# Optimization experiments

Measured on AMD Instinct MI355X. Metric: run time of the kernel, lower is better.

The kernel has to match this reference:

```python
import jax, jax.numpy as jnp
from jax import lax
import numpy as np

WIDTH = 3.0        # tool half-width (voxels)
SIGMA = 1.0        # soft mask edge (voxels)
BLUR_SIGMA = 1.5   # post-deposit isotropic blur sigma (voxels)
EPS = 1e-8


def _gauss_blur(x, sigma):
    """Separable Gaussian blur over the last two axes of x: [B, X, Y]."""
    radius = int(3 * sigma)
    t = jnp.arange(-radius, radius + 1, dtype=x.dtype)
    k = jnp.exp(-0.5 * (t / sigma) ** 2)
    k = k / k.sum()
    x4 = x[:, None]                      # [B,1,X,Y] NCHW
    kh = k.reshape(1, 1, -1, 1)
    x4 = lax.conv_general_dilated(x4, kh, (1, 1), 'SAME')
    kw = k.reshape(1, 1, 1, -1)
    x4 = lax.conv_general_dilated(x4, kw, (1, 1), 'SAME')
    return x4[:, 0]


def setup_inputs() -> dict:
    key = jax.random.key(0)
    k1, k2, k3 = jax.random.split(key, 3)
    B, H, W = 16, 1024, 1024
    occ = jax.random.uniform(k1, (B, H, W), dtype=jnp.float32)
    # push start/end points well inside the grid (voxel coordinates)
    action_start = jax.random.uniform(k2, (B, 3), minval=200.0, maxval=800.0, dtype=jnp.float32)
    action_end = action_start + jax.random.uniform(k3, (B, 3), minval=-150.0, maxval=150.0, dtype=jnp.float32)
    return {"occ": occ, "action_start": action_start, "action_end": action_end}


def reference(occ, action_start, action_end):
    # coordinate-convention transpose (see SplatPushModel docs)
    rho = jnp.swapaxes(occ, 1, 2)            # [B, X, Y]
    B, X, Y = rho.shape
    p0 = action_start[:, :2]                 # [B,2]
    p1 = action_end[:, :2]                   # [B,2]

    d = p1 - p0
    L = jnp.sqrt(jnp.sum(d * d, axis=-1) + EPS)      # [B] segment length
    u = d / L[:, None]                               # unit push direction
    n = jnp.stack([-u[:, 1], u[:, 0]], axis=-1)      # unit normal

    gx = jnp.arange(X, dtype=rho.dtype)[None, :, None]   # [1,X,1]
    gy = jnp.arange(Y, dtype=rho.dtype)[None, None, :]   # [1,1,Y]
    bc = lambda v: v[:, None, None]                      # [B] -> [B,1,1]

    # --- swept band: soft distance-to-segment mask ---
    rx = gx - bc(p0[:, 0])
    ry = gy - bc(p0[:, 1])
    t = jnp.clip(rx * bc(u[:, 0]) + ry * bc(u[:, 1]), 0.0, L[:, None, None])
    dx = rx - t * bc(u[:, 0])
    dy = ry - t * bc(u[:, 1])
    dist = jnp.sqrt(dx * dx + dy * dy + EPS)
    swept = jax.nn.sigmoid((WIDTH - dist) / SIGMA)       # [B,X,Y]

    m_swept = jnp.sum(rho * swept, axis=(1, 2))          # [B] mass to move
    pile_depth = m_swept / (2.0 * WIDTH)                 # [B]

    # --- landing zone probe (rectangle past p1) ---
    qx = gx - bc(p1[:, 0])
    qy = gy - bc(p1[:, 1])
    s = qx * bc(u[:, 0]) + qy * bc(u[:, 1])              # along-direction coord
    r = qx * bc(n[:, 0]) + qy * bc(n[:, 1])              # perpendicular coord
    lat = jax.nn.sigmoid((WIDTH - jnp.abs(r)) / SIGMA)
    probe = jax.nn.sigmoid(s / SIGMA) * jax.nn.sigmoid((bc(pile_depth) - s) / SIGMA) * lat
    existing = jnp.sum(rho * probe, axis=(1, 2))         # [B]
    extra = existing / (2.0 * WIDTH)                     # [B] forward extension

    # --- deposit band, shifted forward by extra_depth ---
    dep_mask = (jax.nn.sigmoid((s - bc(extra)) / SIGMA)
                * jax.nn.sigmoid((bc(extra) + bc(pile_depth) - s) / SIGMA)
                * lat)
    dep_norm = m_swept / (jnp.sum(dep_mask, axis=(1, 2)) + EPS)
    dep = dep_mask * dep_norm[:, None, None]             # mass-conserving deposit

    if BLUR_SIGMA > 0:
        dep = _gauss_blur(dep, BLUR_SIGMA)

    rho_new = rho * (1.0 - swept) + dep
    return jnp.swapaxes(rho_new, 1, 2)
```

## Files before the change

kernel.cpp:

```cpp
#include <hip/hip_runtime.h>
#include <math.h>

#define BB    16
#define HH    1024
#define WW    1024
#define EPSF  1e-8f
#define RAD   4
#define MARG  24.f
#define WMAX  256
#define FW    (WMAX + 16)

struct BlurK { float k[9]; };

__device__ __forceinline__ float sigf(float z) {
    z = fmaxf(fminf(z, 40.f), -40.f);
    return 1.f / (1.f + __expf(-z));
}

struct Geom { float p0x, p0y, p1x, p1y, L, ux, uy; };

__device__ __forceinline__ Geom load_geom(const float* as, const float* ae, int b) {
    Geom g;
    g.p0x = as[3 * b];  g.p0y = as[3 * b + 1];
    g.p1x = ae[3 * b];  g.p1y = ae[3 * b + 1];
    float dx = g.p1x - g.p0x, dy = g.p1y - g.p0y;
    g.L  = sqrtf(dx * dx + dy * dy + EPSF);
    g.ux = dx / g.L;  g.uy = dy / g.L;
    return g;
}

__device__ __forceinline__ float sweptf(const Geom& g, float x, float y) {
    float rx = x - g.p0x, ry = y - g.p0y;
    float t  = fminf(fmaxf(rx * g.ux + ry * g.uy, 0.f), g.L);
    float dx = rx - t * g.ux, dy = ry - t * g.uy;
    float dist = sqrtf(dx * dx + dy * dy + EPSF);
    return sigf(3.f - dist);
}

__device__ __forceinline__ void slat(const Geom& g, float x, float y, float& s, float& lat) {
    float qx = x - g.p1x, qy = y - g.p1y;
    s = qx * g.ux + qy * g.uy;
    float r = qx * (-g.uy) + qy * g.ux;
    lat = sigf(3.f - fabsf(r));
}

__device__ __forceinline__ void capsule_bbox(const Geom& g, float m,
                                             int& x0, int& x1, int& y0, int& y1) {
    x0 = max(0, (int)floorf(fminf(g.p0x, g.p1x) - m));
    x1 = min(WW - 1, (int)ceilf(fmaxf(g.p0x, g.p1x) + m));
    y0 = max(0, (int)floorf(fminf(g.p0y, g.p1y) - m));
    y1 = min(HH - 1, (int)ceilf(fmaxf(g.p0y, g.p1y) + m));
}

__device__ __forceinline__ void strip_bbox(const Geom& g, float s0, float s1, float m,
                                           int& x0, int& x1, int& y0, int& y1) {
    float xmin = 1e9f, xmax = -1e9f, ymin = 1e9f, ymax = -1e9f;
    #pragma unroll
    for (int i = 0; i < 4; i++) {
        float s = (i & 1) ? s1 : s0;
        float r = (i & 2) ? m : -m;
        float x = g.p1x + s * g.ux - r * g.uy;
        float y = g.p1y + s * g.uy + r * g.ux;
        xmin = fminf(xmin, x); xmax = fmaxf(xmax, x);
        ymin = fminf(ymin, y); ymax = fmaxf(ymax, y);
    }
    x0 = max(0, (int)floorf(xmin)); x1 = min(WW - 1, (int)ceilf(xmax));
    y0 = max(0, (int)floorf(ymin)); y1 = min(HH - 1, (int)ceilf(ymax));
}

__device__ __forceinline__ float brb1024(float v, float* sm) {
    #pragma unroll
    for (int off = 32; off > 0; off >>= 1) v += __shfl_down(v, off);
    const int lane = threadIdx.x & 63, wid = threadIdx.x >> 6;
    if (lane == 0) sm[wid] = v;
    __syncthreads();
    float r = 0.f;
    #pragma unroll
    for (int i = 0; i < 16; i++) r += sm[i];
    __syncthreads();
    return r;
}

__global__ __launch_bounds__(1024)
void k_scalars(const float* __restrict__ occ, const float* __restrict__ as,
               const float* __restrict__ ae, float* __restrict__ sc) {
    const int b = blockIdx.x, tid = threadIdx.x;
    const int ty = tid >> 7, tx = tid & 127;
    __shared__ float sm[16];
    Geom g = load_geom(as, ae, b);
    const float* base = occ + ((size_t)b << 20);

    int x0, x1, y0, y1;
    capsule_bbox(g, MARG, x0, x1, y0, y1);
    float sum = 0.f;
    for (int y = y0 + ty; y <= y1; y += 8) {
        const float fy = (float)y;
        for (int x = x0 + tx; x <= x1; x += 128)
            sum += base[((size_t)y << 10) + x] * sweptf(g, (float)x, fy);
    }
    const float m_swept = brb1024(sum, sm);
    const float pile = m_swept * (1.f / 6.f);

    strip_bbox(g, -MARG, pile + MARG, MARG, x0, x1, y0, y1);
    sum = 0.f;
    for (int y = y0 + ty; y <= y1; y += 8) {
        const float fy = (float)y;
        for (int x = x0 + tx; x <= x1; x += 128) {
            float s, lat; slat(g, (float)x, fy, s, lat);
            sum += base[((size_t)y << 10) + x] * sigf(s) * sigf(pile - s) * lat;
        }
    }
    const float existing = brb1024(sum, sm);
    const float extra = existing * (1.f / 6.f);

    strip_bbox(g, extra - MARG, extra + pile + MARG, MARG, x0, x1, y0, y1);
    sum = 0.f;
    for (int y = y0 + ty; y <= y1; y += 8) {
        const float fy = (float)y;
        for (int x = x0 + tx; x <= x1; x += 128) {
            float s, lat; slat(g, (float)x, fy, s, lat);
            sum += sigf(s - extra) * sigf(extra + pile - s) * lat;
        }
    }
    const float summask = brb1024(sum, sm);

    if (tid == 0) {
        sc[b * 4 + 0] = pile;
        sc[b * 4 + 1] = extra;
        sc[b * 4 + 2] = m_swept / (summask + EPSF);
    }
}

__global__ __launch_bounds__(256)
void k_fused(const float* __restrict__ occ, const float* __restrict__ as,
             const float* __restrict__ ae, const float* __restrict__ sc,
             float* __restrict__ out, BlurK wk) {
    const int b = blockIdx.y, bx = blockIdx.x, tid = threadIdx.x;
    const float pile     = sc[b * 4 + 0];
    const float extra    = sc[b * 4 + 1];
    const float dep_norm = sc[b * 4 + 2];
    Geom g = load_geom(as, ae, b);

    const size_t ibase = (size_t)b << 20;
    const float4* src = (const float4*)(occ + ibase);
    float4*       dst = (float4*)(out + ibase);
    const int yb = bx * 8;
    const int base4 = bx * 2048 + tid;

    float4 v[8];
    #pragma unroll
    for (int k = 0; k < 8; k++) v[k] = src[base4 + k * 256];

    int cx0, cx1, cy0, cy1; capsule_bbox(g, MARG, cx0, cx1, cy0, cy1);
    const int x = tid << 2;
    if (x + 3 >= cx0 && x <= cx1) {
        #pragma unroll
        for (int k = 0; k < 8; k++) {
            const int y = yb + k;
            if (y >= cy0 && y <= cy1) {
                const float fy = (float)y, fx = (float)x;
                v[k].x *= 1.f - sweptf(g, fx + 0.f, fy);
                v[k].y *= 1.f - sweptf(g, fx + 1.f, fy);
                v[k].z *= 1.f - sweptf(g, fx + 2.f, fy);
                v[k].w *= 1.f - sweptf(g, fx + 3.f, fy);
            }
        }
    }

    int sx0, sx1, sy0, sy1;
    strip_bbox(g, extra - MARG, extra + pile + MARG, MARG, sx0, sx1, sy0, sy1);

    __shared__ float draw[16][FW];
    __shared__ float hb[16][WMAX];

    if (yb + 7 >= sy0 && yb <= sy1) {
        const int cxa = sx0 & ~3;
        for (int cx = cxa; cx <= sx1; cx += WMAX) {
            const int w = min(WMAX, sx1 - cx + 1);

            for (int i = tid; i < 16 * FW; i += 256) {
                const int ly = i / FW, lx = i - ly * FW;
                if (lx < w + 8) {
                    const int gy = yb - 4 + ly, gx = cx - 4 + lx;
                    float val = 0.f;
                    if ((unsigned)gx < WW && (unsigned)gy < HH) {
                        float s, lat; slat(g, (float)gx, (float)gy, s, lat);
                        val = sigf(s - extra) * sigf(extra + pile - s) * lat * dep_norm;
                    }
                    draw[ly][lx] = val;
                }
            }
            __syncthreads();

            for (int i = tid; i < 16 * WMAX; i += 256) {
                const int ly = i >> 8, lx = i & 255;
                if (lx < w) {
                    float acc = 0.f;
                    #pragma unroll
                    for (int j = 0; j < 9; j++) acc += wk.k[j] * draw[ly][lx + j];
                    hb[ly][lx] = acc;
                }
            }
            __syncthreads();

            for (int i = tid; i < 8 * WMAX; i += 256) {
                const int k = i >> 8, lx = i & 255;
                if (lx < w) {
                    float acc = 0.f;
                    #pragma unroll
                    for (int j = 0; j < 9; j++) acc += wk.k[j] * hb[k + j][lx];
                    draw[k][lx] = acc;
                }
            }
            __syncthreads();

            const int lx0 = (tid << 2) - cx;
            if (lx0 >= 0 && lx0 < w) {
                if (lx0 + 3 < w) {
                    #pragma unroll
                    for (int k = 0; k < 8; k++) {
                        const float4 vb = *(const float4*)&draw[k][lx0];
                        v[k].x += vb.x; v[k].y += vb.y; v[k].z += vb.z; v[k].w += vb.w;
                    }
                } else {
                    #pragma unroll
                    for (int k = 0; k < 8; k++)
                        for (int e = 0; e < 4; e++)
                            if (lx0 + e < w) (&v[k].x)[e] += draw[k][lx0 + e];
                }
            }
            __syncthreads();
        }
    }

    #pragma unroll
    for (int k = 0; k < 8; k++) dst[base4 + k * 256] = v[k];
}

extern "C" void kernel_launch(void* const* d_in, const int* in_sizes, int n_in,
                              void* d_out, int out_size, void* d_ws, size_t ws_size,
                              hipStream_t stream) {
    const float* occ = (const float*)d_in[0];
    const float* as  = (const float*)d_in[1];
    const float* ae  = (const float*)d_in[2];
    float* out = (float*)d_out;
    float* sc  = (float*)d_ws;

    BlurK wk;
    {
        float s = 0.f;
        for (int i = 0; i < 9; i++) {
            float t = (float)(i - RAD) / 1.5f;
            wk.k[i] = expf(-0.5f * t * t);
            s += wk.k[i];
        }
        for (int i = 0; i < 9; i++) wk.k[i] /= s;
    }

    k_scalars<<<dim3(BB), 1024, 0, stream>>>(occ, as, ae, sc);
    k_fused  <<<dim3(HH / 8, BB), 256, 0, stream>>>(occ, as, ae, sc, out, wk);
}
```

Baseline: 167.0 us.

## Tighten deposit blur x-range per row band and vectorize scalar reductions

In the fused kernel, each row band now computes the exact x-interval where the rotated deposit rectangle crosses its 16 halo rows, and only blurs that range. The blur tile width drops from 256 to 128 to cut padded work. In the scalar kernel, the swept and probe reductions now load occ as float4 and unroll four rows, exposing more memory-level parallelism. The intent is to skip blur work on the mostly-empty axis-aligned bounding box and to cut the latency-bound serial scalar kernel, at the cost of per-block interval math and more tile iterations.

```diff
diff --git a/kernel.cpp b/kernel.cpp
--- a/kernel.cpp
+++ b/kernel.cpp
@@ -7,8 +7,9 @@
 #define EPSF  1e-8f
 #define RAD   4
 #define MARG  24.f
-#define WMAX  256
+#define WMAX  128
 #define FW    (WMAX + 16)
+#define UNR   4
 
 struct BlurK { float k[9]; };
 
@@ -68,6 +69,14 @@
     y0 = max(0, (int)floorf(ymin)); y1 = min(HH - 1, (int)ceilf(ymax));
 }
 
+__device__ __forceinline__ bool ivx(float a, float A, float B, float& lo, float& hi) {
+    if (fabsf(a) < 1e-5f) return !(A > 0.f || B < 0.f);
+    float l = A / a, h = B / a;
+    if (a < 0.f) { float t = l; l = h; h = t; }
+    lo = fmaxf(lo, l); hi = fminf(hi, h);
+    return true;
+}
+
 __device__ __forceinline__ float brb1024(float v, float* sm) {
     #pragma unroll
     for (int off = 32; off > 0; off >>= 1) v += __shfl_down(v, off);
@@ -85,29 +94,72 @@
 void k_scalars(const float* __restrict__ occ, const float* __restrict__ as,
                const float* __restrict__ ae, float* __restrict__ sc) {
     const int b = blockIdx.x, tid = threadIdx.x;
-    const int ty = tid >> 7, tx = tid & 127;
+    const int tx4 = tid & 63;
+    const int ty  = tid >> 6;
     __shared__ float sm[16];
     Geom g = load_geom(as, ae, b);
-    const float* base = occ + ((size_t)b << 20);
+    const float4* src4 = (const float4*)(occ + ((size_t)b << 20));
 
     int x0, x1, y0, y1;
+
     capsule_bbox(g, MARG, x0, x1, y0, y1);
+    int c0 = x0 >> 2, c1 = x1 >> 2;
     float sum = 0.f;
-    for (int y = y0 + ty; y <= y1; y += 8) {
-        const float fy = (float)y;
-        for (int x = x0 + tx; x <= x1; x += 128)
-            sum += base[((size_t)y << 10) + x] * sweptf(g, (float)x, fy);
+    for (int cc = c0; cc <= c1; cc += 64) {
+        const int c = cc + tx4;
+        const bool cok = (c <= c1);
+        const float fx = (float)(c << 2);
+        for (int y = y0 + ty; y <= y1; y += 16 * UNR) {
+            float4 vv[UNR];
+            #pragma unroll
+            for (int j = 0; j < UNR; j++) {
+                const int yy = y + 16 * j;
+                vv[j] = (cok && yy <= y1) ? src4[yy * 256 + c]
+                                          : make_float4(0.f, 0.f, 0.f, 0.f);
+            }
+            #pragma unroll
+            for (int j = 0; j < UNR; j++) {
+                const int yy = y + 16 * j;
+                if (cok && yy <= y1) {
+                    const float fy = (float)yy;
+                    sum += vv[j].x * sweptf(g, fx + 0.f, fy);
+                    sum += vv[j].y * sweptf(g, fx + 1.f, fy);
+                    sum += vv[j].z * sweptf(g, fx + 2.f, fy);
+                    sum += vv[j].w * sweptf(g, fx + 3.f, fy);
+                }
+            }
+        }
     }
     const float m_swept = brb1024(sum, sm);
     const float pile = m_swept * (1.f / 6.f);
 
     strip_bbox(g, -MARG, pile + MARG, MARG, x0, x1, y0, y1);
+    c0 = x0 >> 2; c1 = x1 >> 2;
     sum = 0.f;
-    for (int y = y0 + ty; y <= y1; y += 8) {
-        const float fy = (float)y;
-        for (int x = x0 + tx; x <= x1; x += 128) {
-            float s, lat; slat(g, (float)x, fy, s, lat);
-            sum += base[((size_t)y << 10) + x] * sigf(s) * sigf(pile - s) * lat;
+    for (int cc = c0; cc <= c1; cc += 64) {
+        const int c = cc + tx4;
+        const bool cok = (c <= c1);
+        const float fx = (float)(c << 2);
+        for (int y = y0 + ty; y <= y1; y += 16 * UNR) {
+            float4 vv[UNR];
+            #pragma unroll
+            for (int j = 0; j < UNR; j++) {
+                const int yy = y + 16 * j;
+                vv[j] = (cok && yy <= y1) ? src4[yy * 256 + c]
+                                          : make_float4(0.f, 0.f, 0.f, 0.f);
+            }
+            #pragma unroll
+            for (int j = 0; j < UNR; j++) {
+                const int yy = y + 16 * j;
+                if (cok && yy <= y1) {
+                    const float fy = (float)yy;
+                    #pragma unroll
+                    for (int e = 0; e < 4; e++) {
+                        float s, lat; slat(g, fx + (float)e, fy, s, lat);
+                        sum += (&vv[j].x)[e] * sigf(s) * sigf(pile - s) * lat;
+                    }
+                }
+            }
         }
     }
     const float existing = brb1024(sum, sm);
@@ -115,11 +167,14 @@
 
     strip_bbox(g, extra - MARG, extra + pile + MARG, MARG, x0, x1, y0, y1);
     sum = 0.f;
-    for (int y = y0 + ty; y <= y1; y += 8) {
-        const float fy = (float)y;
-        for (int x = x0 + tx; x <= x1; x += 128) {
-            float s, lat; slat(g, (float)x, fy, s, lat);
-            sum += sigf(s - extra) * sigf(extra + pile - s) * lat;
+    {
+        const int tx = tid & 127, ty8 = tid >> 7;
+        for (int y = y0 + ty8; y <= y1; y += 8) {
+            const float fy = (float)y;
+            for (int x = x0 + tx; x <= x1; x += 128) {
+                float s, lat; slat(g, (float)x, fy, s, lat);
+                sum += sigf(s - extra) * sigf(extra + pile - s) * lat;
+            }
         }
     }
     const float summask = brb1024(sum, sm);
@@ -174,62 +229,77 @@
     __shared__ float hb[16][WMAX];
 
     if (yb + 7 >= sy0 && yb <= sy1) {
-        const int cxa = sx0 & ~3;
-        for (int cx = cxa; cx <= sx1; cx += WMAX) {
-            const int w = min(WMAX, sx1 - cx + 1);
-
-            for (int i = tid; i < 16 * FW; i += 256) {
-                const int ly = i / FW, lx = i - ly * FW;
-                if (lx < w + 8) {
-                    const int gy = yb - 4 + ly, gx = cx - 4 + lx;
-                    float val = 0.f;
-                    if ((unsigned)gx < WW && (unsigned)gy < HH) {
-                        float s, lat; slat(g, (float)gx, (float)gy, s, lat);
-                        val = sigf(s - extra) * sigf(extra + pile - s) * lat * dep_norm;
-                    }
-                    draw[ly][lx] = val;
-                }
-            }
-            __syncthreads();
-
-            for (int i = tid; i < 16 * WMAX; i += 256) {
-                const int ly = i >> 8, lx = i & 255;
-                if (lx < w) {
-                    float acc = 0.f;
-                    #pragma unroll
-                    for (int j = 0; j < 9; j++) acc += wk.k[j] * draw[ly][lx + j];
-                    hb[ly][lx] = acc;
-                }
-            }
-            __syncthreads();
-
-            for (int i = tid; i < 8 * WMAX; i += 256) {
-                const int k = i >> 8, lx = i & 255;
-                if (lx < w) {
-                    float acc = 0.f;
-                    #pragma unroll
-                    for (int j = 0; j < 9; j++) acc += wk.k[j] * hb[k + j][lx];
-                    draw[k][lx] = acc;
-                }
-            }
-            __syncthreads();
-
-            const int lx0 = (tid << 2) - cx;
-            if (lx0 >= 0 && lx0 < w) {
-                if (lx0 + 3 < w) {
-                    #pragma unroll
-                    for (int k = 0; k < 8; k++) {
-                        const float4 vb = *(const float4*)&draw[k][lx0];
-                        v[k].x += vb.x; v[k].y += vb.y; v[k].z += vb.z; v[k].w += vb.w;
-                    }
-                } else {
-                    #pragma unroll
-                    for (int k = 0; k < 8; k++)
-                        for (int e = 0; e < 4; e++)
-                            if (lx0 + e < w) (&v[k].x)[e] += draw[k][lx0 + e];
-                }
-            }
-            __syncthreads();
+        const float sA = extra - MARG, sB = extra + pile + MARG;
+        float xlo = 1e9f, xhi = -1e9f;
+        #pragma unroll
+        for (int r = 0; r < 16; r++) {
+            const float dy = (float)(yb - RAD + r) - g.p1y;
+            float lo = -1e9f, hi = 1e9f;
+            bool ok = ivx(g.ux, sA - dy * g.uy, sB - dy * g.uy, lo, hi);
+            ok = ok && ivx(-g.uy, -MARG - dy * g.ux, MARG - dy * g.ux, lo, hi);
+            if (ok && lo <= hi) { xlo = fminf(xlo, lo); xhi = fmaxf(xhi, hi); }
+        }
+        const int csx0 = max(sx0, (int)floorf(xlo + g.p1x));
+        const int csx1 = min(sx1, (int)ceilf(xhi + g.p1x));
+
+        if (csx0 <= csx1) {
+            const int cxa = csx0 & ~3;
+            for (int cx = cxa; cx <= csx1; cx += WMAX) {
+                const int w = min(WMAX, csx1 - cx + 1);
+
+                for (int i = tid; i < 16 * FW; i += 256) {
+                    const int ly = i / FW, lx = i - ly * FW;
+                    if (lx < w + 8) {
+                        const int gy = yb - RAD + ly, gx = cx - RAD + lx;
+                        float val = 0.f;
+                        if ((unsigned)gx < WW && (unsigned)gy < HH) {
+                            float s, lat; slat(g, (float)gx, (float)gy, s, lat);
+                            val = sigf(s - extra) * sigf(extra + pile - s) * lat * dep_norm;
+                        }
+                        draw[ly][lx] = val;
+                    }
+                }
+                __syncthreads();
+
+                for (int i = tid; i < 16 * WMAX; i += 256) {
+                    const int ly = i >> 7, lx = i & 127;
+                    if (lx < w) {
+                        float acc = 0.f;
+                        #pragma unroll
+                        for (int j = 0; j < 9; j++) acc += wk.k[j] * draw[ly][lx + j];
+                        hb[ly][lx] = acc;
+                    }
+                }
+                __syncthreads();
+
+                for (int i = tid; i < 8 * WMAX; i += 256) {
+                    const int k = i >> 7, lx = i & 127;
+                    if (lx < w) {
+                        float acc = 0.f;
+                        #pragma unroll
+                        for (int j = 0; j < 9; j++) acc += wk.k[j] * hb[k + j][lx];
+                        draw[k][lx] = acc;
+                    }
+                }
+                __syncthreads();
+
+                const int lx0 = (tid << 2) - cx;
+                if (lx0 >= 0 && lx0 < w) {
+                    if (lx0 + 3 < w) {
+                        #pragma unroll
+                        for (int k = 0; k < 8; k++) {
+                            const float4 vb = *(const float4*)&draw[k][lx0];
+                            v[k].x += vb.x; v[k].y += vb.y; v[k].z += vb.z; v[k].w += vb.w;
+                        }
+                    } else {
+                        #pragma unroll
+                        for (int k = 0; k < 8; k++)
+                            for (int e = 0; e < 4; e++)
+                                if (lx0 + e < w) (&v[k].x)[e] += draw[k][lx0 + e];
+                    }
+                }
+                __syncthreads();
+            }
         }
     }
 
```

Result: faster. 163.3 us (-2.2%).
